# Kernel optimization log

Hardware: AMD Instinct MI355X
Metric: run time of the kernel (lower is better)

The kernel has to match this reference:

```python
import jax, jax.numpy as jnp
import numpy as np

NA, NM, NT = 4353, 3676, 8000
N = NA + NM + NT
E = 500000
S = 200000
D_IN, DP, DE, DC, HID = 512, 256, 128, 64, 16


def setup_inputs() -> dict:
    key = jax.random.key(0)
    ks = jax.random.split(key, 32)
    f = lambda k, shp, s: (jax.random.normal(k, shp, jnp.float32) * s)
    inp = {
        'h_author': f(ks[0], (NA, D_IN), 1.0),
        'h_movie': f(ks[1], (NM, D_IN), 1.0),
        'h_term': f(ks[2], (NT, D_IN), 1.0),
        'Wp_author': f(ks[3], (D_IN, DP), D_IN ** -0.5),
        'Wp_movie': f(ks[4], (D_IN, DP), D_IN ** -0.5),
        'Wp_term': f(ks[5], (D_IN, DP), D_IN ** -0.5),
        'W1': f(ks[6], (DP, DE), DP ** -0.5),
        'b1': jnp.zeros((DE,), jnp.float32),
        'W2': f(ks[7], (DE, DE), DE ** -0.5),
        'b2': jnp.zeros((DE,), jnp.float32),
        'Wc_author': f(ks[8], (DE, DC), DE ** -0.5),
        'Wc_movie': f(ks[9], (DE, DC), DE ** -0.5),
        'Wc_term': f(ks[10], (DE, DC), DE ** -0.5),
        'Wh_author': f(ks[11], (DE + 2 * DC, HID), (DE + 2 * DC) ** -0.5),
        'Wh_movie': f(ks[12], (DE + 2 * DC, HID), (DE + 2 * DC) ** -0.5),
        'Wh_term': f(ks[13], (DE + 2 * DC, HID), (DE + 2 * DC) ** -0.5),
        'Wo_author': f(ks[14], (HID, 1), HID ** -0.5),
        'Wo_movie': f(ks[15], (HID, 1), HID ** -0.5),
        'Wo_term': f(ks[16], (HID, 1), HID ** -0.5),
        'src': jax.random.randint(ks[17], (E,), 0, N),
        'dst': jax.random.randint(ks[18], (E,), 0, N),
        'ns0_author': jax.random.randint(ks[19], (S,), 0, NA),
        'ns0_movie': jax.random.randint(ks[20], (S,), 0, NM),
        'ns0_term': jax.random.randint(ks[21], (S,), 0, NT),
        'ns1_author': jax.random.randint(ks[22], (S,), 0, NA),
        'ns1_movie': jax.random.randint(ks[23], (S,), 0, NM),
        'ns1_term': jax.random.randint(ks[24], (S,), 0, NT),
        'ns2_author': jax.random.randint(ks[25], (S,), 0, NA),
        'ns2_movie': jax.random.randint(ks[26], (S,), 0, NM),
        'ns2_term': jax.random.randint(ks[27], (S,), 0, NT),
    }
    return inp


def reference(h_author, h_movie, h_term, Wp_author, Wp_movie, Wp_term,
              W1, b1, W2, b2, Wc_author, Wc_movie, Wc_term,
              Wh_author, Wh_movie, Wh_term, Wo_author, Wo_movie, Wo_term,
              src, dst, ns0_author, ns0_movie, ns0_term,
              ns1_author, ns1_movie, ns1_term, ns2_author, ns2_movie, ns2_term):
    # per-ntype feature projection (bias=False), concat in ntype order -> homogeneous [N, DP]
    H = jnp.concatenate([h_author @ Wp_author, h_movie @ Wp_movie, h_term @ Wp_term], axis=0)
    # GraphConv(norm='none'): out = (sum over in-edges of src feat) @ W + b
    agg1 = jax.ops.segment_sum(H[src], dst, num_segments=N)      # [N, DP]
    h1 = jax.nn.relu(agg1 @ W1 + b1)                             # [N, DE]
    agg2 = jax.ops.segment_sum(h1[src], dst, num_segments=N)    # [N, DE]
    h2 = agg2 @ W2 + b2
    # F.normalize(p=2, dim=1, eps=1e-12)
    h = h2 / jnp.maximum(jnp.linalg.norm(h2, axis=1, keepdims=True), 1e-12)
    ha, hm, ht = h[:NA], h[NA:NA + NM], h[NA + NM:]
    # per-ntype context encoder (bias=False)
    ca, cm, ct = ha @ Wc_author, hm @ Wc_movie, ht @ Wc_term

    def cls(feat, Wh, Wo):
        return jax.nn.relu(feat @ Wh) @ Wo  # multi_2Linear, bias=False

    # target emb first, then context of other ntypes in ntype order
    t0 = jnp.concatenate([ha[ns0_author], cm[ns0_movie], ct[ns0_term]], axis=1)
    t1 = jnp.concatenate([hm[ns1_movie], ca[ns1_author], ct[ns1_term]], axis=1)
    t2 = jnp.concatenate([ht[ns2_term], ca[ns2_author], cm[ns2_movie]], axis=1)
    p = jnp.concatenate([cls(t0, Wh_author, Wo_author),
                         cls(t1, Wh_movie, Wo_movie),
                         cls(t2, Wh_term, Wo_term)], axis=0)
    x = jax.nn.sigmoid(p).ravel()
    out_h_movie = h[4353:8029]
    return h, x, out_h_movie
```

## Files before the change

kernel.cpp:

```cpp
#include <hip/hip_runtime.h>
#include <hip/hip_bf16.h>

namespace {
constexpr int kNA = 4353, kNM = 3676, kNT = 8000;
constexpr int kN  = kNA + kNM + kNT;
constexpr int kE  = 500000;
constexpr int kS  = 200000;
constexpr int kDIN = 512, kDP = 256, kDE = 128, kDC = 64;

constexpr size_t OUT_X  = (size_t)kN * kDE;
constexpr size_t OUT_HM = OUT_X + 3ull * kS;

constexpr size_t align256(size_t x) { return (x + 255) & ~size_t(255); }

constexpr size_t OFF_WPW1 = 0;
constexpr size_t OFF_M9   = OFF_WPW1 + 3ull * 512 * 128 * 4;
constexpr size_t OFF_HW1  = align256(OFF_M9 + 9ull * 2048 * 4);
constexpr size_t OFF_H1   = OFF_HW1 + (size_t)kN * kDE * 4;
constexpr size_t OFF_AGG2 = OFF_H1  + (size_t)kN * kDE * 4;
constexpr size_t OFF_HN   = OFF_AGG2 + (size_t)kN * kDE * 4;
constexpr size_t OFF_P    = OFF_HN  + (size_t)kN * kDE * 4;
constexpr size_t OFF_ESRC = align256(OFF_P + 3ull * kN * 16 * 4);
constexpr size_t OFF_RP   = align256(OFF_ESRC + (size_t)kE * 4);
constexpr size_t OFF_CUR  = align256(OFF_RP + (size_t)(kN + 1) * 4);
constexpr size_t WS_NEEDED = align256(OFF_CUR + (size_t)kN * 4);

constexpr int kBA = (kNA + 15) / 16;
constexpr int kBM = (kNM + 15) / 16;
constexpr int kBT = (kNT + 15) / 16;
constexpr int kHW1Blocks = kBA + kBM + kBT;
constexpr int kG2Blocks  = (kN + 15) / 16;
}

__global__ __launch_bounds__(128) void prep1_kernel(
    const float* __restrict__ WpA, const float* __restrict__ WpM,
    const float* __restrict__ WpT, const float* __restrict__ W1,
    float* __restrict__ WpW1)
{
    int b = blockIdx.x;
    int t = b >> 7;
    int k0 = (b & 127) * 4;
    const float* Wp = (t == 0) ? WpA : ((t == 1) ? WpM : WpT);
    int c = threadIdx.x;
    float acc[4] = {0.f, 0.f, 0.f, 0.f};
    for (int j = 0; j < kDP; j++) {
        float w1 = W1[j * kDE + c];
#pragma unroll
        for (int r = 0; r < 4; r++)
            acc[r] += Wp[(k0 + r) * kDP + j] * w1;
    }
#pragma unroll
    for (int r = 0; r < 4; r++)
        WpW1[((size_t)t * kDIN + k0 + r) * kDE + c] = acc[r];
}

__global__ __launch_bounds__(256) void prep2_kernel(
    const float* __restrict__ WhA, const float* __restrict__ WhM,
    const float* __restrict__ WhT,
    const float* __restrict__ WcA, const float* __restrict__ WcM,
    const float* __restrict__ WcT,
    float* __restrict__ M9)
{
    int b = blockIdx.x;
    int g = b / 3, t = b % 3;
    const float* Wh = (g == 0) ? WhA : ((g == 1) ? WhM : WhT);
    const float* Wc = (t == 0) ? WcA : ((t == 1) ? WcM : WcT);
    int slot;
    if (t == g) slot = 0;
    else {
        int lower = (g == 0) ? 1 : 0;
        slot = (t == lower) ? 128 : 192;
    }
    float* Mout = M9 + (size_t)b * 2048;
    for (int idx = threadIdx.x; idx < 2048; idx += 256) {
        int k = idx >> 4, j = idx & 15;
        float v;
        if (slot == 0) v = Wh[k * 16 + j];
        else {
            v = 0.f;
            for (int d = 0; d < kDC; d++)
                v += Wc[k * kDC + d] * Wh[(slot + d) * 16 + j];
        }
        Mout[idx] = v;
    }
}

__global__ __launch_bounds__(256) void hw1_kernel(
    const float* __restrict__ hA, const float* __restrict__ hM,
    const float* __restrict__ hT, const float* __restrict__ WpW1,
    float* __restrict__ HW1)
{
    __shared__ float AL[16 * kDIN];
    int b = blockIdx.x;
    const float *A, *W; int typeN, rowBase, lb;
    if (b < kBA)             { lb = b;             A = hA; W = WpW1;                   typeN = kNA; rowBase = 0; }
    else if (b < kBA + kBM)  { lb = b - kBA;       A = hM; W = WpW1 + 1ull*kDIN*kDE;   typeN = kNM; rowBase = kNA; }
    else                     { lb = b - kBA - kBM; A = hT; W = WpW1 + 2ull*kDIN*kDE;   typeN = kNT; rowBase = kNA + kNM; }
    int r0 = lb * 16;

    const float4* Ag = (const float4*)A;
#pragma unroll
    for (int i = 0; i < 8; i++) {
        int f = threadIdx.x + i * 256;
        int rl = f >> 7, k4 = f & 127;
        int gr = min(r0 + rl, typeN - 1);
        ((float4*)AL)[f] = Ag[(size_t)gr * 128 + k4];
    }
    __syncthreads();

    int col = threadIdx.x & 127;
    int hh  = threadIdx.x >> 7;
    const float* ALh = AL + hh * 8 * kDIN;
    float acc[8];
#pragma unroll
    for (int r = 0; r < 8; r++) acc[r] = 0.f;

    for (int k0 = 0; k0 < kDIN; k0 += 8) {
        float w[8];
#pragma unroll
        for (int i = 0; i < 8; i++)
            w[i] = W[(size_t)(k0 + i) * kDE + col];
#pragma unroll
        for (int r = 0; r < 8; r++) {
            const float4 a0 = *(const float4*)(ALh + r * kDIN + k0);
            const float4 a1 = *(const float4*)(ALh + r * kDIN + k0 + 4);
            acc[r] += a0.x * w[0] + a0.y * w[1] + a0.z * w[2] + a0.w * w[3]
                    + a1.x * w[4] + a1.y * w[5] + a1.z * w[6] + a1.w * w[7];
        }
    }
#pragma unroll
    for (int r = 0; r < 8; r++) {
        int lr = r0 + hh * 8 + r;
        if (lr < typeN) HW1[(size_t)(rowBase + lr) * kDE + col] = acc[r];
    }
}

__device__ __forceinline__ int clampN(int v) { return min(max(v, 0), kN - 1); }

__global__ __launch_bounds__(256) void hist_kernel(const int* __restrict__ key,
                                                   int* __restrict__ counts)
{
    int e = blockIdx.x * 256 + threadIdx.x;
    if (e < kE) atomicAdd(&counts[clampN(key[e])], 1);
}

__global__ __launch_bounds__(256) void scan_kernel(int* __restrict__ cnt_cur,
                                                   int* __restrict__ rowptr)
{
    __shared__ int sums[256];
    int tid = threadIdx.x;
    int i0 = tid * 63, i1 = min(i0 + 63, kN);
    int s = 0;
    for (int i = i0; i < i1; i++) s += cnt_cur[i];
    sums[tid] = s;
    __syncthreads();
    if (tid == 0) {
        int run = 0;
        for (int i = 0; i < 256; i++) { int v = sums[i]; sums[i] = run; run += v; }
    }
    __syncthreads();
    int base = sums[tid];
    for (int i = i0; i < i1; i++) {
        int c = cnt_cur[i];
        rowptr[i] = base;
        cnt_cur[i] = base;
        base += c;
    }
    if (tid == 0) rowptr[kN] = kE;
}

__global__ __launch_bounds__(256) void fill_kernel(const int* __restrict__ stored,
                                                   const int* __restrict__ key,
                                                   int* __restrict__ cursor,
                                                   int* __restrict__ esrc)
{
    int e = blockIdx.x * 256 + threadIdx.x;
    if (e < kE) {
        int p = atomicAdd(&cursor[clampN(key[e])], 1);
        esrc[min(p, kE - 1)] = clampN(stored[e]);
    }
}

template <bool RELU>
__global__ __launch_bounds__(64) void aggv_kernel(const float* __restrict__ X,
                                                  const int* __restrict__ rowptr,
                                                  const int* __restrict__ esrc,
                                                  const float* __restrict__ b1,
                                                  float* __restrict__ out)
{
    int n = blockIdx.x;
    int lane = threadIdx.x;
    int eo = lane >> 5;
    int cg = lane & 31;
    int start = rowptr[n], end = rowptr[n + 1];
    const float4* X4 = (const float4*)X;
    float4 a0 = {0.f, 0.f, 0.f, 0.f}, a1 = {0.f, 0.f, 0.f, 0.f};
    int j = start + eo;
    for (; j + 2 < end; j += 4) {
        int s0 = esrc[j];
        int s1 = esrc[j + 2];
        float4 v0 = X4[(size_t)s0 * 32 + cg];
        float4 v1 = X4[(size_t)s1 * 32 + cg];
        a0.x += v0.x; a0.y += v0.y; a0.z += v0.z; a0.w += v0.w;
        a1.x += v1.x; a1.y += v1.y; a1.z += v1.z; a1.w += v1.w;
    }
    if (j < end) {
        float4 v0 = X4[(size_t)esrc[j] * 32 + cg];
        a0.x += v0.x; a0.y += v0.y; a0.z += v0.z; a0.w += v0.w;
    }
    float4 acc;
    acc.x = a0.x + a1.x; acc.y = a0.y + a1.y;
    acc.z = a0.z + a1.z; acc.w = a0.w + a1.w;
    acc.x += __shfl_xor(acc.x, 32);
    acc.y += __shfl_xor(acc.y, 32);
    acc.z += __shfl_xor(acc.z, 32);
    acc.w += __shfl_xor(acc.w, 32);
    if (lane < 32) {
        if (RELU) {
            const float4 bv = ((const float4*)b1)[cg];
            acc.x = fmaxf(acc.x + bv.x, 0.f);
            acc.y = fmaxf(acc.y + bv.y, 0.f);
            acc.z = fmaxf(acc.z + bv.z, 0.f);
            acc.w = fmaxf(acc.w + bv.w, 0.f);
        }
        ((float4*)out)[(size_t)n * 32 + cg] = acc;
    }
}

__global__ __launch_bounds__(256) void gemm2_norm_kernel(
    const float* __restrict__ X, const float* __restrict__ W2,
    const float* __restrict__ b2, float* __restrict__ hn,
    float* __restrict__ out)
{
    __shared__ float AL[16 * kDE];
    __shared__ float red[16][2];
    int r0 = blockIdx.x * 16;

    const float4* Xg = (const float4*)X;
#pragma unroll
    for (int i = 0; i < 2; i++) {
        int f = threadIdx.x + i * 256;
        int rl = f >> 5, k4 = f & 31;
        int gr = min(r0 + rl, kN - 1);
        ((float4*)AL)[f] = Xg[(size_t)gr * 32 + k4];
    }
    __syncthreads();

    int col = threadIdx.x & 127;
    int hh  = threadIdx.x >> 7;
    const float* ALh = AL + hh * 8 * kDE;
    float acc[8];
#pragma unroll
    for (int r = 0; r < 8; r++) acc[r] = 0.f;

    for (int k0 = 0; k0 < kDE; k0 += 8) {
        float w[8];
#pragma unroll
        for (int i = 0; i < 8; i++)
            w[i] = W2[(size_t)(k0 + i) * kDE + col];
#pragma unroll
        for (int r = 0; r < 8; r++) {
            const float4 a0 = *(const float4*)(ALh + r * kDE + k0);
            const float4 a1 = *(const float4*)(ALh + r * kDE + k0 + 4);
            acc[r] += a0.x * w[0] + a0.y * w[1] + a0.z * w[2] + a0.w * w[3]
                    + a1.x * w[4] + a1.y * w[5] + a1.z * w[6] + a1.w * w[7];
        }
    }

    float bv = b2[col];
    int half = (threadIdx.x >> 6) & 1;
#pragma unroll
    for (int r = 0; r < 8; r++) {
        float v = acc[r] + bv;
        acc[r] = v;
        float ss = v * v;
#pragma unroll
        for (int o = 32; o > 0; o >>= 1) ss += __shfl_xor(ss, o);
        if ((threadIdx.x & 63) == 0) red[hh * 8 + r][half] = ss;
    }
    __syncthreads();
#pragma unroll
    for (int r = 0; r < 8; r++) {
        int gr = r0 + hh * 8 + r;
        if (gr < kN) {
            float tot = red[hh * 8 + r][0] + red[hh * 8 + r][1];
            float sc = 1.f / fmaxf(sqrtf(tot), 1e-12f);
            float hv = acc[r] * sc;
            hn[(size_t)gr * kDE + col] = hv;
            out[(size_t)gr * kDE + col] = hv;
            if (gr >= kNA && gr < kNA + kNM)
                out[OUT_HM + (size_t)(gr - kNA) * kDE + col] = hv;
        }
    }
}

__global__ __launch_bounds__(128) void partial_kernel(const float* __restrict__ hn,
                                                      const float* __restrict__ M9,
                                                      float* __restrict__ P)
{
    __shared__ float HL[8 * 132];
    int b = blockIdx.x;
    int g = b / 2005, b2 = b % 2005;
    int t, lb, typeN, rowBase;
    if (b2 < 545)       { t = 0; lb = b2;        typeN = kNA; rowBase = 0; }
    else if (b2 < 1005) { t = 1; lb = b2 - 545;  typeN = kNM; rowBase = kNA; }
    else                { t = 2; lb = b2 - 1005; typeN = kNT; rowBase = kNA + kNM; }
    int tid = threadIdx.x;
    const float4* hn4 = (const float4*)hn;
#pragma unroll
    for (int i = 0; i < 2; i++) {
        int f = tid + i * 128;
        int rl = f >> 5, k4 = f & 31;
        int gr = min(lb * 8 + rl, typeN - 1);
        *(float4*)(HL + rl * 132 + k4 * 4) = hn4[(size_t)(rowBase + gr) * 32 + k4];
    }
    __syncthreads();

    int r = tid >> 4, j = tid & 15;
    int lr = lb * 8 + r;
    if (lr >= typeN) return;
    const float* M = M9 + (size_t)(g * 3 + t) * 2048;
    const float* Hr = HL + r * 132;
    float acc = 0.f;
    for (int k = 0; k < kDE; k += 4) {
        const float4 h4 = *(const float4*)(Hr + k);
        acc += h4.x * M[(k + 0) * 16 + j] + h4.y * M[(k + 1) * 16 + j]
             + h4.z * M[(k + 2) * 16 + j] + h4.w * M[(k + 3) * 16 + j];
    }
    P[((size_t)g * kN + rowBase + lr) * 16 + j] = acc;
}

__global__ __launch_bounds__(256) void cls_lite_kernel(
    const float* __restrict__ P,
    const int* __restrict__ n0a, const int* __restrict__ n0m, const int* __restrict__ n0t,
    const int* __restrict__ n1a, const int* __restrict__ n1m, const int* __restrict__ n1t,
    const int* __restrict__ n2a, const int* __restrict__ n2m, const int* __restrict__ n2t,
    const float* __restrict__ WoA, const float* __restrict__ WoM, const float* __restrict__ WoT,
    float* __restrict__ out, int blocksPerGroup)
{
    int g = blockIdx.x / blocksPerGroup;
    int i = (blockIdx.x % blocksPerGroup) * 256 + threadIdx.x;
    if (i >= kS) return;
    auto cA = [](int v){ return min(max(v, 0), kNA - 1); };
    auto cM = [](int v){ return min(max(v, 0), kNM - 1); };
    auto cT = [](int v){ return min(max(v, 0), kNT - 1); };
    int ra, rb, rc;
    if (g == 0)      { ra = cA(n0a[i]);             rb = kNA + cM(n0m[i]);  rc = kNA + kNM + cT(n0t[i]); }
    else if (g == 1) { ra = kNA + cM(n1m[i]);       rb = cA(n1a[i]);        rc = kNA + kNM + cT(n1t[i]); }
    else             { ra = kNA + kNM + cT(n2t[i]); rb = cA(n2a[i]);        rc = kNA + cM(n2m[i]); }
    const float* Pg = P + (size_t)g * kN * 16;
    const float* wo = (g == 0) ? WoA : ((g == 1) ? WoM : WoT);
    const float4* pa = (const float4*)(Pg + (size_t)ra * 16);
    const float4* pb = (const float4*)(Pg + (size_t)rb * 16);
    const float4* pc = (const float4*)(Pg + (size_t)rc * 16);
    float p = 0.f;
#pragma unroll
    for (int q = 0; q < 4; q++) {
        float4 a = pa[q], b = pb[q], c = pc[q];
        p += fmaxf(a.x + b.x + c.x, 0.f) * wo[q * 4 + 0];
        p += fmaxf(a.y + b.y + c.y, 0.f) * wo[q * 4 + 1];
        p += fmaxf(a.z + b.z + c.z, 0.f) * wo[q * 4 + 2];
        p += fmaxf(a.w + b.w + c.w, 0.f) * wo[q * 4 + 3];
    }
    out[OUT_X + (size_t)g * kS + i] = 1.f / (1.f + expf(-p));
}

extern "C" void kernel_launch(void* const* d_in, const int* in_sizes, int n_in,
                              void* d_out, int out_size, void* d_ws, size_t ws_size,
                              hipStream_t stream)
{
    (void)out_size;
    static const int expected[30] = {
        2228736, 1882112, 4096000, 131072, 131072, 131072, 32768, 128, 16384, 128,
        8192, 8192, 8192, 4096, 4096, 4096, 16, 16, 16,
        500000, 500000, 200000, 200000, 200000, 200000, 200000, 200000, 200000, 200000, 200000 };
    if (n_in != 30) return;
    for (int i = 0; i < 30; i++) if (in_sizes[i] != expected[i]) return;
    if (ws_size < WS_NEEDED) return;

    const float* h_a  = (const float*)d_in[0];
    const float* h_m  = (const float*)d_in[1];
    const float* h_t  = (const float*)d_in[2];
    const float* Wp_a = (const float*)d_in[3];
    const float* Wp_m = (const float*)d_in[4];
    const float* Wp_t = (const float*)d_in[5];
    const float* W1   = (const float*)d_in[6];
    const float* b1   = (const float*)d_in[7];
    const float* W2   = (const float*)d_in[8];
    const float* b2   = (const float*)d_in[9];
    const float* Wc_a = (const float*)d_in[10];
    const float* Wc_m = (const float*)d_in[11];
    const float* Wc_t = (const float*)d_in[12];
    const float* Wh_a = (const float*)d_in[13];
    const float* Wh_m = (const float*)d_in[14];
    const float* Wh_t = (const float*)d_in[15];
    const float* Wo_a = (const float*)d_in[16];
    const float* Wo_m = (const float*)d_in[17];
    const float* Wo_t = (const float*)d_in[18];
    const int* src = (const int*)d_in[19];
    const int* dst = (const int*)d_in[20];

    char* ws = (char*)d_ws;
    float* WpW1  = (float*)(ws + OFF_WPW1);
    float* M9    = (float*)(ws + OFF_M9);
    float* HW1   = (float*)(ws + OFF_HW1);
    float* h1    = (float*)(ws + OFF_H1);
    float* agg2  = (float*)(ws + OFF_AGG2);
    float* hn    = (float*)(ws + OFF_HN);
    float* P     = (float*)(ws + OFF_P);
    int* esrc    = (int*)(ws + OFF_ESRC);
    int* rowptr  = (int*)(ws + OFF_RP);
    int* cursor  = (int*)(ws + OFF_CUR);
    float* out   = (float*)d_out;

    hipMemsetAsync(cursor, 0, (size_t)kN * 4, stream);

    hist_kernel<<<dim3(1954), dim3(256), 0, stream>>>(dst, cursor);
    scan_kernel<<<dim3(1), dim3(256), 0, stream>>>(cursor, rowptr);
    fill_kernel<<<dim3(1954), dim3(256), 0, stream>>>(src, dst, cursor, esrc);

    prep1_kernel<<<dim3(384), dim3(128), 0, stream>>>(Wp_a, Wp_m, Wp_t, W1, WpW1);
    prep2_kernel<<<dim3(9), dim3(256), 0, stream>>>(Wh_a, Wh_m, Wh_t, Wc_a, Wc_m, Wc_t, M9);

    hw1_kernel<<<dim3(kHW1Blocks), dim3(256), 0, stream>>>(h_a, h_m, h_t, WpW1, HW1);
    aggv_kernel<true><<<dim3(kN), dim3(64), 0, stream>>>(HW1, rowptr, esrc, b1, h1);
    aggv_kernel<false><<<dim3(kN), dim3(64), 0, stream>>>(h1, rowptr, esrc, b1, agg2);
    gemm2_norm_kernel<<<dim3(kG2Blocks), dim3(256), 0, stream>>>(agg2, W2, b2, hn, out);
    partial_kernel<<<dim3(6015), dim3(128), 0, stream>>>(hn, M9, P);
    cls_lite_kernel<<<dim3(2346), dim3(256), 0, stream>>>(P,
        (const int*)d_in[21], (const int*)d_in[22], (const int*)d_in[23],
        (const int*)d_in[24], (const int*)d_in[25], (const int*)d_in[26],
        (const int*)d_in[27], (const int*)d_in[28], (const int*)d_in[29],
        Wo_a, Wo_m, Wo_t, out, 782);
}
```

Before: 303.9 us.

## Store aggregation intermediates in bf16 and fuse partial projection into normalize kernel

The HW1 and h1 intermediates are now stored as bf16, which halves the bytes moved by the two edge-gather aggregation kernels. The partial classifier projection is fused into the GEMM2+normalize kernel, reusing the normalized rows kept in shared memory and dropping the hn buffer and one launch. The two weight-prep kernels are merged into one launch. The cost is reduced precision on gathered features and fewer, larger per-block workloads in the fused kernel.

After: 262.7 us. -13.5%, faster.

```diff
diff --git a/kernel.cpp b/kernel.cpp
--- a/kernel.cpp
+++ b/kernel.cpp
@@ -15,11 +15,10 @@
 
 constexpr size_t OFF_WPW1 = 0;
 constexpr size_t OFF_M9   = OFF_WPW1 + 3ull * 512 * 128 * 4;
-constexpr size_t OFF_HW1  = align256(OFF_M9 + 9ull * 2048 * 4);
-constexpr size_t OFF_H1   = OFF_HW1 + (size_t)kN * kDE * 4;
-constexpr size_t OFF_AGG2 = OFF_H1  + (size_t)kN * kDE * 4;
-constexpr size_t OFF_HN   = OFF_AGG2 + (size_t)kN * kDE * 4;
-constexpr size_t OFF_P    = OFF_HN  + (size_t)kN * kDE * 4;
+constexpr size_t OFF_HW1B = align256(OFF_M9 + 9ull * 2048 * 4);
+constexpr size_t OFF_H1B  = align256(OFF_HW1B + (size_t)kN * kDE * 2);
+constexpr size_t OFF_AGG2 = align256(OFF_H1B + (size_t)kN * kDE * 2);
+constexpr size_t OFF_P    = align256(OFF_AGG2 + (size_t)kN * kDE * 4);
 constexpr size_t OFF_ESRC = align256(OFF_P + 3ull * kN * 16 * 4);
 constexpr size_t OFF_RP   = align256(OFF_ESRC + (size_t)kE * 4);
 constexpr size_t OFF_CUR  = align256(OFF_RP + (size_t)(kN + 1) * 4);
@@ -32,63 +31,71 @@
 constexpr int kG2Blocks  = (kN + 15) / 16;
 }
 
-__global__ __launch_bounds__(128) void prep1_kernel(
+__device__ __forceinline__ float blo(unsigned u) { return __uint_as_float(u << 16); }
+__device__ __forceinline__ float bhi(unsigned u) { return __uint_as_float(u & 0xffff0000u); }
+__device__ __forceinline__ unsigned short b16(float f) {
+    __hip_bfloat16 h = __float2bfloat16(f);
+    return *reinterpret_cast<unsigned short*>(&h);
+}
+__device__ __forceinline__ unsigned pack2(float a, float b) {
+    return (unsigned)b16(a) | ((unsigned)b16(b) << 16);
+}
+
+__global__ __launch_bounds__(128) void prep_kernel(
     const float* __restrict__ WpA, const float* __restrict__ WpM,
     const float* __restrict__ WpT, const float* __restrict__ W1,
-    float* __restrict__ WpW1)
-{
-    int b = blockIdx.x;
-    int t = b >> 7;
-    int k0 = (b & 127) * 4;
-    const float* Wp = (t == 0) ? WpA : ((t == 1) ? WpM : WpT);
-    int c = threadIdx.x;
-    float acc[4] = {0.f, 0.f, 0.f, 0.f};
-    for (int j = 0; j < kDP; j++) {
-        float w1 = W1[j * kDE + c];
-#pragma unroll
-        for (int r = 0; r < 4; r++)
-            acc[r] += Wp[(k0 + r) * kDP + j] * w1;
-    }
-#pragma unroll
-    for (int r = 0; r < 4; r++)
-        WpW1[((size_t)t * kDIN + k0 + r) * kDE + c] = acc[r];
-}
-
-__global__ __launch_bounds__(256) void prep2_kernel(
     const float* __restrict__ WhA, const float* __restrict__ WhM,
     const float* __restrict__ WhT,
     const float* __restrict__ WcA, const float* __restrict__ WcM,
     const float* __restrict__ WcT,
-    float* __restrict__ M9)
+    float* __restrict__ WpW1, float* __restrict__ M9)
 {
     int b = blockIdx.x;
-    int g = b / 3, t = b % 3;
-    const float* Wh = (g == 0) ? WhA : ((g == 1) ? WhM : WhT);
-    const float* Wc = (t == 0) ? WcA : ((t == 1) ? WcM : WcT);
-    int slot;
-    if (t == g) slot = 0;
-    else {
-        int lower = (g == 0) ? 1 : 0;
-        slot = (t == lower) ? 128 : 192;
-    }
-    float* Mout = M9 + (size_t)b * 2048;
-    for (int idx = threadIdx.x; idx < 2048; idx += 256) {
-        int k = idx >> 4, j = idx & 15;
-        float v;
-        if (slot == 0) v = Wh[k * 16 + j];
+    if (b < 384) {
+        int t = b >> 7;
+        int k0 = (b & 127) * 4;
+        const float* Wp = (t == 0) ? WpA : ((t == 1) ? WpM : WpT);
+        int c = threadIdx.x;
+        float acc[4] = {0.f, 0.f, 0.f, 0.f};
+        for (int j = 0; j < kDP; j++) {
+            float w1 = W1[j * kDE + c];
+#pragma unroll
+            for (int r = 0; r < 4; r++)
+                acc[r] += Wp[(k0 + r) * kDP + j] * w1;
+        }
+#pragma unroll
+        for (int r = 0; r < 4; r++)
+            WpW1[((size_t)t * kDIN + k0 + r) * kDE + c] = acc[r];
+    } else {
+        int b2 = b - 384;
+        int g = b2 / 3, t = b2 % 3;
+        const float* Wh = (g == 0) ? WhA : ((g == 1) ? WhM : WhT);
+        const float* Wc = (t == 0) ? WcA : ((t == 1) ? WcM : WcT);
+        int slot;
+        if (t == g) slot = 0;
         else {
-            v = 0.f;
-            for (int d = 0; d < kDC; d++)
-                v += Wc[k * kDC + d] * Wh[(slot + d) * 16 + j];
-        }
-        Mout[idx] = v;
+            int lower = (g == 0) ? 1 : 0;
+            slot = (t == lower) ? 128 : 192;
+        }
+        float* Mout = M9 + (size_t)b2 * 2048;
+        for (int idx = threadIdx.x; idx < 2048; idx += 128) {
+            int k = idx >> 4, j = idx & 15;
+            float v;
+            if (slot == 0) v = Wh[k * 16 + j];
+            else {
+                v = 0.f;
+                for (int d = 0; d < kDC; d++)
+                    v += Wc[k * kDC + d] * Wh[(slot + d) * 16 + j];
+            }
+            Mout[idx] = v;
+        }
     }
 }
 
 __global__ __launch_bounds__(256) void hw1_kernel(
     const float* __restrict__ hA, const float* __restrict__ hM,
     const float* __restrict__ hT, const float* __restrict__ WpW1,
-    float* __restrict__ HW1)
+    __hip_bfloat16* __restrict__ HW1b)
 {
     __shared__ float AL[16 * kDIN];
     int b = blockIdx.x;
@@ -131,7 +138,7 @@
 #pragma unroll
     for (int r = 0; r < 8; r++) {
         int lr = r0 + hh * 8 + r;
-        if (lr < typeN) HW1[(size_t)(rowBase + lr) * kDE + col] = acc[r];
+        if (lr < typeN) HW1b[(size_t)(rowBase + lr) * kDE + col] = __float2bfloat16(acc[r]);
     }
 }
 
@@ -181,32 +188,30 @@
     }
 }
 
-template <bool RELU>
-__global__ __launch_bounds__(64) void aggv_kernel(const float* __restrict__ X,
+template <bool FIRST>
+__global__ __launch_bounds__(64) void aggv_kernel(const __hip_bfloat16* __restrict__ Xb,
                                                   const int* __restrict__ rowptr,
                                                   const int* __restrict__ esrc,
                                                   const float* __restrict__ b1,
-                                                  float* __restrict__ out)
+                                                  void* __restrict__ outv)
 {
     int n = blockIdx.x;
     int lane = threadIdx.x;
     int eo = lane >> 5;
     int cg = lane & 31;
     int start = rowptr[n], end = rowptr[n + 1];
-    const float4* X4 = (const float4*)X;
+    const uint2* X2 = (const uint2*)Xb;
     float4 a0 = {0.f, 0.f, 0.f, 0.f}, a1 = {0.f, 0.f, 0.f, 0.f};
     int j = start + eo;
     for (; j + 2 < end; j += 4) {
-        int s0 = esrc[j];
-        int s1 = esrc[j + 2];
-        float4 v0 = X4[(size_t)s0 * 32 + cg];
-        float4 v1 = X4[(size_t)s1 * 32 + cg];
-        a0.x += v0.x; a0.y += v0.y; a0.z += v0.z; a0.w += v0.w;
-        a1.x += v1.x; a1.y += v1.y; a1.z += v1.z; a1.w += v1.w;
+        uint2 v0 = X2[(size_t)esrc[j] * 32 + cg];
+        uint2 v1 = X2[(size_t)esrc[j + 2] * 32 + cg];
+        a0.x += blo(v0.x); a0.y += bhi(v0.x); a0.z += blo(v0.y); a0.w += bhi(v0.y);
+        a1.x += blo(v1.x); a1.y += bhi(v1.x); a1.z += blo(v1.y); a1.w += bhi(v1.y);
     }
     if (j < end) {
-        float4 v0 = X4[(size_t)esrc[j] * 32 + cg];
-        a0.x += v0.x; a0.y += v0.y; a0.z += v0.z; a0.w += v0.w;
+        uint2 v0 = X2[(size_t)esrc[j] * 32 + cg];
+        a0.x += blo(v0.x); a0.y += bhi(v0.x); a0.z += blo(v0.y); a0.w += bhi(v0.y);
     }
     float4 acc;
     acc.x = a0.x + a1.x; acc.y = a0.y + a1.y;
@@ -216,21 +221,26 @@
     acc.z += __shfl_xor(acc.z, 32);
     acc.w += __shfl_xor(acc.w, 32);
     if (lane < 32) {
-        if (RELU) {
+        if (FIRST) {
             const float4 bv = ((const float4*)b1)[cg];
             acc.x = fmaxf(acc.x + bv.x, 0.f);
             acc.y = fmaxf(acc.y + bv.y, 0.f);
             acc.z = fmaxf(acc.z + bv.z, 0.f);
             acc.w = fmaxf(acc.w + bv.w, 0.f);
-        }
-        ((float4*)out)[(size_t)n * 32 + cg] = acc;
-    }
-}
-
-__global__ __launch_bounds__(256) void gemm2_norm_kernel(
+            uint2 o;
+            o.x = pack2(acc.x, acc.y);
+            o.y = pack2(acc.z, acc.w);
+            ((uint2*)outv)[(size_t)n * 32 + cg] = o;
+        } else {
+            ((float4*)outv)[(size_t)n * 32 + cg] = acc;
+        }
+    }
+}
+
+__global__ __launch_bounds__(256) void gemm2_norm_p_kernel(
     const float* __restrict__ X, const float* __restrict__ W2,
-    const float* __restrict__ b2, float* __restrict__ hn,
-    float* __restrict__ out)
+    const float* __restrict__ b2, const float* __restrict__ M9,
+    float* __restrict__ P, float* __restrict__ out)
 {
     __shared__ float AL[16 * kDE];
     __shared__ float red[16][2];
@@ -281,53 +291,36 @@
     __syncthreads();
 #pragma unroll
     for (int r = 0; r < 8; r++) {
-        int gr = r0 + hh * 8 + r;
+        int lrow = hh * 8 + r;
+        int gr = r0 + lrow;
         if (gr < kN) {
-            float tot = red[hh * 8 + r][0] + red[hh * 8 + r][1];
+            float tot = red[lrow][0] + red[lrow][1];
             float sc = 1.f / fmaxf(sqrtf(tot), 1e-12f);
             float hv = acc[r] * sc;
-            hn[(size_t)gr * kDE + col] = hv;
+            AL[lrow * kDE + col] = hv;
             out[(size_t)gr * kDE + col] = hv;
             if (gr >= kNA && gr < kNA + kNM)
                 out[OUT_HM + (size_t)(gr - kNA) * kDE + col] = hv;
         }
     }
-}
-
-__global__ __launch_bounds__(128) void partial_kernel(const float* __restrict__ hn,
-                                                      const float* __restrict__ M9,
-                                                      float* __restrict__ P)
-{
-    __shared__ float HL[8 * 132];
-    int b = blockIdx.x;
-    int g = b / 2005, b2 = b % 2005;
-    int t, lb, typeN, rowBase;
-    if (b2 < 545)       { t = 0; lb = b2;        typeN = kNA; rowBase = 0; }
-    else if (b2 < 1005) { t = 1; lb = b2 - 545;  typeN = kNM; rowBase = kNA; }
-    else                { t = 2; lb = b2 - 1005; typeN = kNT; rowBase = kNA + kNM; }
-    int tid = threadIdx.x;
-    const float4* hn4 = (const float4*)hn;
-#pragma unroll
-    for (int i = 0; i < 2; i++) {
-        int f = tid + i * 128;
-        int rl = f >> 5, k4 = f & 31;
-        int gr = min(lb * 8 + rl, typeN - 1);
-        *(float4*)(HL + rl * 132 + k4 * 4) = hn4[(size_t)(rowBase + gr) * 32 + k4];
-    }
-    __syncthreads();
-
-    int r = tid >> 4, j = tid & 15;
-    int lr = lb * 8 + r;
-    if (lr >= typeN) return;
-    const float* M = M9 + (size_t)(g * 3 + t) * 2048;
-    const float* Hr = HL + r * 132;
-    float acc = 0.f;
-    for (int k = 0; k < kDE; k += 4) {
-        const float4 h4 = *(const float4*)(Hr + k);
-        acc += h4.x * M[(k + 0) * 16 + j] + h4.y * M[(k + 1) * 16 + j]
-             + h4.z * M[(k + 2) * 16 + j] + h4.w * M[(k + 3) * 16 + j];
-    }
-    P[((size_t)g * kN + rowBase + lr) * 16 + j] = acc;
+    __syncthreads();
+
+    int r = threadIdx.x >> 4, j = threadIdx.x & 15;
+    int gr = r0 + r;
+    if (gr >= kN) return;
+    int t = (gr < kNA) ? 0 : ((gr < kNA + kNM) ? 1 : 2);
+    const float* Hr = AL + r * kDE;
+#pragma unroll
+    for (int g = 0; g < 3; g++) {
+        const float* M = M9 + (size_t)(g * 3 + t) * 2048;
+        float acc2 = 0.f;
+        for (int k = 0; k < kDE; k += 4) {
+            const float4 h4 = *(const float4*)(Hr + k);
+            acc2 += h4.x * M[(k + 0) * 16 + j] + h4.y * M[(k + 1) * 16 + j]
+                  + h4.z * M[(k + 2) * 16 + j] + h4.w * M[(k + 3) * 16 + j];
+        }
+        P[((size_t)g * kN + gr) * 16 + j] = acc2;
+    }
 }
 
 __global__ __launch_bounds__(256) void cls_lite_kernel(
@@ -401,17 +394,16 @@
     const int* dst = (const int*)d_in[20];
 
     char* ws = (char*)d_ws;
-    float* WpW1  = (float*)(ws + OFF_WPW1);
-    float* M9    = (float*)(ws + OFF_M9);
-    float* HW1   = (float*)(ws + OFF_HW1);
-    float* h1    = (float*)(ws + OFF_H1);
-    float* agg2  = (float*)(ws + OFF_AGG2);
-    float* hn    = (float*)(ws + OFF_HN);
-    float* P     = (float*)(ws + OFF_P);
-    int* esrc    = (int*)(ws + OFF_ESRC);
-    int* rowptr  = (int*)(ws + OFF_RP);
-    int* cursor  = (int*)(ws + OFF_CUR);
-    float* out   = (float*)d_out;
+    float* WpW1 = (float*)(ws + OFF_WPW1);
+    float* M9   = (float*)(ws + OFF_M9);
+    __hip_bfloat16* HW1b = (__hip_bfloat16*)(ws + OFF_HW1B);
+    __hip_bfloat16* h1b  = (__hip_bfloat16*)(ws + OFF_H1B);
+    float* agg2 = (float*)(ws + OFF_AGG2);
+    float* P    = (float*)(ws + OFF_P);
+    int* esrc   = (int*)(ws + OFF_ESRC);
+    int* rowptr = (int*)(ws + OFF_RP);
+    int* cursor = (int*)(ws + OFF_CUR);
+    float* out  = (float*)d_out;
 
     hipMemsetAsync(cursor, 0, (size_t)kN * 4, stream);
 
@@ -419,14 +411,13 @@
     scan_kernel<<<dim3(1), dim3(256), 0, stream>>>(cursor, rowptr);
     fill_kernel<<<dim3(1954), dim3(256), 0, stream>>>(src, dst, cursor, esrc);
 
-    prep1_kernel<<<dim3(384), dim3(128), 0, stream>>>(Wp_a, Wp_m, Wp_t, W1, WpW1);
-    prep2_kernel<<<dim3(9), dim3(256), 0, stream>>>(Wh_a, Wh_m, Wh_t, Wc_a, Wc_m, Wc_t, M9);
-
-    hw1_kernel<<<dim3(kHW1Blocks), dim3(256), 0, stream>>>(h_a, h_m, h_t, WpW1, HW1);
-    aggv_kernel<true><<<dim3(kN), dim3(64), 0, stream>>>(HW1, rowptr, esrc, b1, h1);
-    aggv_kernel<false><<<dim3(kN), dim3(64), 0, stream>>>(h1, rowptr, esrc, b1, agg2);
-    gemm2_norm_kernel<<<dim3(kG2Blocks), dim3(256), 0, stream>>>(agg2, W2, b2, hn, out);
-    partial_kernel<<<dim3(6015), dim3(128), 0, stream>>>(hn, M9, P);
+    prep_kernel<<<dim3(393), dim3(128), 0, stream>>>(Wp_a, Wp_m, Wp_t, W1,
+        Wh_a, Wh_m, Wh_t, Wc_a, Wc_m, Wc_t, WpW1, M9);
+
+    hw1_kernel<<<dim3(kHW1Blocks), dim3(256), 0, stream>>>(h_a, h_m, h_t, WpW1, HW1b);
+    aggv_kernel<true><<<dim3(kN), dim3(64), 0, stream>>>(HW1b, rowptr, esrc, b1, h1b);
+    aggv_kernel<false><<<dim3(kN), dim3(64), 0, stream>>>(h1b, rowptr, esrc, b1, agg2);
+    gemm2_norm_p_kernel<<<dim3(kG2Blocks), dim3(256), 0, stream>>>(agg2, W2, b2, M9, P, out);
     cls_lite_kernel<<<dim3(2346), dim3(256), 0, stream>>>(P,
         (const int*)d_in[21], (const int*)d_in[22], (const int*)d_in[23],
         (const int*)d_in[24], (const int*)d_in[25], (const int*)d_in[26],
```
